# Kernel tuning notes

Measured on AMD Instinct MI355X. Metric: run time of the kernel, lower is better.

## Reference

```python
import jax, jax.numpy as jnp
import numpy as np


def setup_inputs() -> dict:
    key = jax.random.key(0)
    kq, kk, kv = jax.random.split(key, 3)
    B, H, S, D = 2, 16, 2048, 128
    return {
        "query_states": jax.random.normal(kq, (B, H, S, D), dtype=jnp.float32),
        "key_states": jax.random.normal(kk, (B, H, S, D), dtype=jnp.float32),
        "value_states": jax.random.normal(kv, (B, H, S, D), dtype=jnp.float32),
    }


def reference(query_states, key_states, value_states):
    # Faithful translation of CoreAttention.forward with attention_mask=None,
    # attention_dropout=0.0 (default, and dropout with p=0 is identity).
    B, H, Sq, D = query_states.shape
    Skv = key_states.shape[-2]
    scale = 1.0 / jnp.sqrt(jnp.asarray(D, dtype=query_states.dtype))
    # [B,H,Sq,Skv] score matrix (the module materializes this explicitly)
    attn_weights = jnp.einsum("bhqd,bhkd->bhqk", query_states, key_states) * scale
    # internal causal mask: triu(ones, diagonal=1) positions -> dtype min
    causal = jnp.triu(jnp.ones((Sq, Skv), dtype=bool), k=1)
    mask_value = jnp.finfo(attn_weights.dtype).min
    attn_weights = jnp.where(causal[None, None], mask_value, attn_weights)
    # torch does softmax in float64 then casts back; numerically stable fp32
    # softmax is equivalent to working precision here (jax x64 disabled).
    attn_weights = jax.nn.softmax(attn_weights, axis=-1).astype(query_states.dtype)
    attn_output = jnp.einsum("bhqk,bhkd->bhqd", attn_weights, value_states)
    return attn_output
```

## Files before the change

### kernel.cpp

```cpp
#include <hip/hip_runtime.h>
#include <hip/hip_bf16.h>
#include <stdint.h>

typedef __bf16  bf16x8 __attribute__((ext_vector_type(8)));
typedef __bf16  bf16x4 __attribute__((ext_vector_type(4)));
typedef float   f32x4  __attribute__((ext_vector_type(4)));
typedef uint32_t u32x4 __attribute__((ext_vector_type(4)));

#define S     2048
#define D     128
#define KVBLK 32
#define NQT   32
#define THR2  11.5415603f

__device__ __forceinline__ uint32_t cvt_pk(float lo, float hi2) {
    uint32_t u;
    asm("v_cvt_pk_bf16_f32 %0, %1, %2" : "=v"(u) : "v"(lo), "v"(hi2));
    return u;
}
__device__ __forceinline__ float exp2fast(float x) {
    return __builtin_amdgcn_exp2f(x);
}
__device__ __forceinline__ void gl2lds16(const void* g, void* l) {
    __builtin_amdgcn_global_load_lds(
        (const __attribute__((address_space(1))) void*)g,
        (__attribute__((address_space(3))) void*)l, 16, 0, 0);
}

__global__ __launch_bounds__(256) void pack_kv(
    const float* __restrict__ K, const float* __restrict__ V,
    __bf16* __restrict__ Kp, __bf16* __restrict__ Vp)
{
    const int bh = blockIdx.x, t = blockIdx.y;
    const int tid = threadIdx.x;
    const int kv0 = t * KVBLK;

    {
        const float* src = K + ((size_t)bh * S + kv0) * D;
        char* dst = (char*)Kp + ((size_t)(bh * 64 + t)) * 8192;
        #pragma unroll
        for (int cc = 0; cc < 2; ++cc) {
            const int c = cc * 256 + tid;
            const int row = c >> 4, col16 = c & 15;
            const float4 a = *reinterpret_cast<const float4*>(src + row * D + col16 * 8);
            const float4 b = *reinterpret_cast<const float4*>(src + row * D + col16 * 8 + 4);
            bf16x8 o;
            o[0]=(__bf16)a.x; o[1]=(__bf16)a.y; o[2]=(__bf16)a.z; o[3]=(__bf16)a.w;
            o[4]=(__bf16)b.x; o[5]=(__bf16)b.y; o[6]=(__bf16)b.z; o[7]=(__bf16)b.w;
            *reinterpret_cast<bf16x8*>(
                dst + row * 256 + ((col16 * 16) ^ ((row & 15) << 4))) = o;
        }
    }

    __shared__ __bf16 lds[32][136];
    {
        const float* src = V + ((size_t)bh * S + kv0) * D;
        #pragma unroll
        for (int it = 0; it < 4; ++it) {
            const int id = it * 256 + tid;
            const int row = id >> 5, c4 = id & 31;
            float4 v = *reinterpret_cast<const float4*>(src + row * D + c4 * 4);
            bf16x4 b4;
            b4[0]=(__bf16)v.x; b4[1]=(__bf16)v.y; b4[2]=(__bf16)v.z; b4[3]=(__bf16)v.w;
            *reinterpret_cast<bf16x4*>(&lds[row][c4 * 4]) = b4;
        }
    }
    __syncthreads();
    {
        char* dst = (char*)Vp + ((size_t)(bh * 64 + t)) * 8192;
        #pragma unroll
        for (int cc = 0; cc < 2; ++cc) {
            const int c = cc * 256 + tid;
            const int d = c >> 2, c8 = c & 3;
            bf16x8 o;
            #pragma unroll
            for (int k = 0; k < 8; ++k) o[k] = lds[c8 * 8 + k][d];
            const int addr = (d >> 1) * 128 +
                ((((d & 1) << 6) + c8 * 16) ^ (((d >> 1) & 3) << 4));
            *reinterpret_cast<bf16x8*>(dst + addr) = o;
        }
    }
}

__global__ __launch_bounds__(256, 4) void attn_fwd(
    const float* __restrict__ Q, const __bf16* __restrict__ Kp,
    const __bf16* __restrict__ Vp, float* __restrict__ O)
{
    const int bh = blockIdx.x;
    const int qt = (NQT - 1) - blockIdx.y;
    const int tid  = threadIdx.x;
    const int w    = tid >> 6;
    const int lane = tid & 63;
    const int r    = lane & 15;
    const int g    = lane >> 4;

    const float* Qh = Q + (size_t)bh * S * D;
    float*       Oh = O + (size_t)bh * S * D;
    const char*  Kbase = (const char*)Kp + (size_t)bh * 64 * 8192;
    const char*  Vbase = (const char*)Vp + (size_t)bh * 64 * 8192;

    const int q0w = qt * 64 + w * 16;

    __shared__ __align__(16) __bf16 K_sh[2][KVBLK * D];
    __shared__ __align__(16) __bf16 V_sh[2][D * KVBLK];

    const float scale = 0.08838834764831845f * 1.4426950408889634f;

    bf16x8 qfrag[4];
    {
        const float4* qp = reinterpret_cast<const float4*>(
            Qh + (size_t)(q0w + r) * D + g * 8);
        #pragma unroll
        for (int kb = 0; kb < 4; ++kb) {
            float4 a = qp[kb*8 + 0];
            float4 b = qp[kb*8 + 1];
            a.x*=scale; a.y*=scale; a.z*=scale; a.w*=scale;
            b.x*=scale; b.y*=scale; b.z*=scale; b.w*=scale;
            bf16x8 f;
            f[0]=(__bf16)a.x; f[1]=(__bf16)a.y; f[2]=(__bf16)a.z; f[3]=(__bf16)a.w;
            f[4]=(__bf16)b.x; f[5]=(__bf16)b.y; f[6]=(__bf16)b.z; f[7]=(__bf16)b.w;
            qfrag[kb] = f;
        }
    }

    auto STAGE = [&](int buf, int t) {
        const char* ks = Kbase + (size_t)t * 8192 + w * 1024 + lane * 16;
        const char* vs = Vbase + (size_t)t * 8192 + w * 1024 + lane * 16;
        char* kd = (char*)(&K_sh[buf][0]) + w * 1024;
        char* vd = (char*)(&V_sh[buf][0]) + w * 1024;
        gl2lds16(ks,        kd);
        gl2lds16(ks + 4096, kd + 4096);
        gl2lds16(vs,        vd);
        gl2lds16(vs + 4096, vd + 4096);
    };

    const f32x4 vzero = {0.f, 0.f, 0.f, 0.f};
    f32x4 acc_o[8];
    #pragma unroll
    for (int i = 0; i < 8; ++i) acc_o[i] = vzero;
    float m_run = -1e30f, l_run = 0.f;

    const int n_iter = 2 * qt + 2;
    const int my_max = (q0w + 15) >> 5;

    STAGE(0, 0);
    __syncthreads();
    int cur = 0;

    for (int t = 0; t < n_iter; ++t) {
        if (t + 1 < n_iter) STAGE(cur ^ 1, t + 1);

        if (t <= my_max) {
            const int kv0 = t * KVBLK;
            char* Kb = reinterpret_cast<char*>(&K_sh[cur][0]);
            char* Vb = reinterpret_cast<char*>(&V_sh[cur][0]);
            const bool alive1 = (kv0 + 16 <= q0w + 15);

            f32x4 st[2] = {vzero, vzero};
            __builtin_amdgcn_s_setprio(1);
            #pragma unroll
            for (int tt = 0; tt < 2; ++tt) {
                if (tt == 1 && !alive1) break;
                const int row = tt * 16 + r;
                #pragma unroll
                for (int kb = 0; kb < 4; ++kb) {
                    bf16x8 kf = *reinterpret_cast<const bf16x8*>(
                        Kb + row * 256 + ((kb*64 + g*16) ^ ((row & 15) << 4)));
                    st[tt] = __builtin_amdgcn_mfma_f32_16x16x32_bf16(
                        kf, qfrag[kb], st[tt], 0, 0, 0);
                }
            }
            __builtin_amdgcn_s_setprio(0);

            const int q = q0w + r;
            float pmax = -1e30f;
            #pragma unroll
            for (int tt = 0; tt < 2; ++tt) {
                if (tt == 1 && !alive1) break;
                if (kv0 + tt*16 + 15 > q0w) {
                    #pragma unroll
                    for (int jj = 0; jj < 4; ++jj)
                        if (kv0 + tt*16 + 4*g + jj > q) st[tt][jj] = -1e30f;
                }
                #pragma unroll
                for (int jj = 0; jj < 4; ++jj) pmax = fmaxf(pmax, st[tt][jj]);
            }
            pmax = fmaxf(pmax, __shfl_xor(pmax, 16));
            pmax = fmaxf(pmax, __shfl_xor(pmax, 32));

            if (__any(pmax > m_run + THR2)) {
                const float m_new = fmaxf(m_run, pmax);
                const float corr  = exp2fast(m_run - m_new);
                l_run *= corr; m_run = m_new;
                #pragma unroll
                for (int reg = 0; reg < 4; ++reg) {
                    const float cr = __shfl(corr, 4*g + reg);
                    #pragma unroll
                    for (int dt = 0; dt < 8; ++dt) acc_o[dt][reg] *= cr;
                }
            }

            float rowsum = 0.f;
            #pragma unroll
            for (int tt = 0; tt < 2; ++tt) {
                if (tt == 1 && !alive1) break;
                #pragma unroll
                for (int jj = 0; jj < 4; ++jj) {
                    const float p = exp2fast(st[tt][jj] - m_run);
                    st[tt][jj] = p;
                    rowsum += p;
                }
            }
            rowsum += __shfl_xor(rowsum, 16);
            rowsum += __shfl_xor(rowsum, 32);
            l_run += rowsum;

            const uint32_t p00 = cvt_pk(st[0][0], st[0][1]);
            const uint32_t p01 = cvt_pk(st[0][2], st[0][3]);
            const uint32_t p10 = alive1 ? cvt_pk(st[1][0], st[1][1]) : 0u;
            const uint32_t p11 = alive1 ? cvt_pk(st[1][2], st[1][3]) : 0u;
            const int sA = r + ((2 * (g & 1)) << 4);
            const int sB = r + ((2 * (g & 1) + 1) << 4);
            u32x4 words;
            {
                const uint32_t lo0 = (uint32_t)__shfl((int)p00, sA);
                const uint32_t hi0 = (uint32_t)__shfl((int)p10, sA);
                const uint32_t lo1 = (uint32_t)__shfl((int)p01, sA);
                const uint32_t hi1 = (uint32_t)__shfl((int)p11, sA);
                const uint32_t lo2 = (uint32_t)__shfl((int)p00, sB);
                const uint32_t hi2 = (uint32_t)__shfl((int)p10, sB);
                const uint32_t lo3 = (uint32_t)__shfl((int)p01, sB);
                const uint32_t hi3 = (uint32_t)__shfl((int)p11, sB);
                words[0] = (g & 2) ? hi0 : lo0;
                words[1] = (g & 2) ? hi1 : lo1;
                words[2] = (g & 2) ? hi2 : lo2;
                words[3] = (g & 2) ? hi3 : lo3;
            }
            const bf16x8 pa = __builtin_bit_cast(bf16x8, words);

            __builtin_amdgcn_s_setprio(1);
            #pragma unroll
            for (int dt = 0; dt < 8; ++dt) {
                const int d = dt * 16 + r;
                const int byte = (d >> 1) * 128 +
                    ((((d & 1) << 6) + (g << 4)) ^ (((d >> 1) & 3) << 4));
                bf16x8 vf = *reinterpret_cast<const bf16x8*>(Vb + byte);
                acc_o[dt] = __builtin_amdgcn_mfma_f32_16x16x32_bf16(
                    pa, vf, acc_o[dt], 0, 0, 0);
            }
            __builtin_amdgcn_s_setprio(0);
        }

        __syncthreads();
        cur ^= 1;
    }

    const float inv = 1.0f / l_run;
    #pragma unroll
    for (int reg = 0; reg < 4; ++reg) {
        const float iv = __shfl(inv, 4*g + reg);
        float* orow = Oh + (size_t)(q0w + 4*g + reg) * D + r;
        #pragma unroll
        for (int dt = 0; dt < 8; ++dt)
            orow[dt * 16] = acc_o[dt][reg] * iv;
    }
}

extern "C" void kernel_launch(void* const* d_in, const int* in_sizes, int n_in,
                              void* d_out, int out_size, void* d_ws, size_t ws_size,
                              hipStream_t stream) {
    const float* Q = (const float*)d_in[0];
    const float* K = (const float*)d_in[1];
    const float* V = (const float*)d_in[2];
    float* O = (float*)d_out;

    __bf16* Kp = (__bf16*)d_ws;
    __bf16* Vp = Kp + (size_t)32 * S * D;

    pack_kv<<<dim3(32, 64), 256, 0, stream>>>(K, V, Kp, Vp);
    attn_fwd<<<dim3(32, NQT), 256, 0, stream>>>(Q, Kp, Vp, O);
}
```

Baseline: 104.2 us.

## Pair high and low causal query tiles per block to balance work

Each block now handles two query tiles, one from the top and one from the bottom of the causal triangle. Both share each staged K/V tile from shared memory, so every block does roughly equal work and K/V loads are reused across the pair. The grid is halved and launch bounds drop to 2 waves per SIMD to make room for the doubled accumulators. The trade is lower occupancy and fewer blocks in exchange for load balance and less K/V traffic.

After: 104.9 us. Within noise of the previous version (+0.7%).

```diff
diff --git a/kernel.cpp b/kernel.cpp
--- a/kernel.cpp
+++ b/kernel.cpp
@@ -82,12 +82,14 @@
     }
 }
 
-__global__ __launch_bounds__(256, 4) void attn_fwd(
+__global__ __launch_bounds__(256, 2) void attn_fwd(
     const float* __restrict__ Q, const __bf16* __restrict__ Kp,
     const __bf16* __restrict__ Vp, float* __restrict__ O)
 {
     const int bh = blockIdx.x;
-    const int qt = (NQT - 1) - blockIdx.y;
+    const int y  = blockIdx.y;
+    const int qtH = NQT - 1 - y;
+    const int qtL = y;
     const int tid  = threadIdx.x;
     const int w    = tid >> 6;
     const int lane = tid & 63;
@@ -99,17 +101,17 @@
     const char*  Kbase = (const char*)Kp + (size_t)bh * 64 * 8192;
     const char*  Vbase = (const char*)Vp + (size_t)bh * 64 * 8192;
 
-    const int q0w = qt * 64 + w * 16;
+    const int q0H = qtH * 64 + w * 16;
+    const int q0L = qtL * 64 + w * 16;
 
     __shared__ __align__(16) __bf16 K_sh[2][KVBLK * D];
     __shared__ __align__(16) __bf16 V_sh[2][D * KVBLK];
 
     const float scale = 0.08838834764831845f * 1.4426950408889634f;
 
-    bf16x8 qfrag[4];
-    {
+    auto load_q = [&](int q0, bf16x8* qf) {
         const float4* qp = reinterpret_cast<const float4*>(
-            Qh + (size_t)(q0w + r) * D + g * 8);
+            Qh + (size_t)(q0 + r) * D + g * 8);
         #pragma unroll
         for (int kb = 0; kb < 4; ++kb) {
             float4 a = qp[kb*8 + 0];
@@ -119,9 +121,12 @@
             bf16x8 f;
             f[0]=(__bf16)a.x; f[1]=(__bf16)a.y; f[2]=(__bf16)a.z; f[3]=(__bf16)a.w;
             f[4]=(__bf16)b.x; f[5]=(__bf16)b.y; f[6]=(__bf16)b.z; f[7]=(__bf16)b.w;
-            qfrag[kb] = f;
-        }
-    }
+            qf[kb] = f;
+        }
+    };
+    bf16x8 qfH[4], qfL[4];
+    load_q(q0H, qfH);
+    load_q(q0L, qfL);
 
     auto STAGE = [&](int buf, int t) {
         const char* ks = Kbase + (size_t)t * 8192 + w * 1024 + lane * 16;
@@ -135,13 +140,115 @@
     };
 
     const f32x4 vzero = {0.f, 0.f, 0.f, 0.f};
-    f32x4 acc_o[8];
+    f32x4 accH[8], accL[8];
     #pragma unroll
-    for (int i = 0; i < 8; ++i) acc_o[i] = vzero;
-    float m_run = -1e30f, l_run = 0.f;
-
-    const int n_iter = 2 * qt + 2;
-    const int my_max = (q0w + 15) >> 5;
+    for (int i = 0; i < 8; ++i) { accH[i] = vzero; accL[i] = vzero; }
+    float mH = -1e30f, lH = 0.f, mL = -1e30f, lL = 0.f;
+
+    const int n_iter = 2 * qtH + 2;
+    const int maxH = (q0H + 15) >> 5;
+    const int maxL = (q0L + 15) >> 5;
+
+    auto stream_tile = [&](int t, int q0, const bf16x8* qf,
+                           f32x4* acc, float& m_run, float& l_run,
+                           char* Kb, char* Vb) {
+        const int kv0 = t * KVBLK;
+        const bool alive1 = (kv0 + 16 <= q0 + 15);
+
+        f32x4 st[2] = {vzero, vzero};
+        __builtin_amdgcn_s_setprio(1);
+        #pragma unroll
+        for (int tt = 0; tt < 2; ++tt) {
+            if (tt == 1 && !alive1) break;
+            const int row = tt * 16 + r;
+            #pragma unroll
+            for (int kb = 0; kb < 4; ++kb) {
+                bf16x8 kf = *reinterpret_cast<const bf16x8*>(
+                    Kb + row * 256 + ((kb*64 + g*16) ^ ((row & 15) << 4)));
+                st[tt] = __builtin_amdgcn_mfma_f32_16x16x32_bf16(
+                    kf, qf[kb], st[tt], 0, 0, 0);
+            }
+        }
+        __builtin_amdgcn_s_setprio(0);
+
+        const int q = q0 + r;
+        float pmax = -1e30f;
+        #pragma unroll
+        for (int tt = 0; tt < 2; ++tt) {
+            if (tt == 1 && !alive1) break;
+            if (kv0 + tt*16 + 15 > q0) {
+                #pragma unroll
+                for (int jj = 0; jj < 4; ++jj)
+                    if (kv0 + tt*16 + 4*g + jj > q) st[tt][jj] = -1e30f;
+            }
+            #pragma unroll
+            for (int jj = 0; jj < 4; ++jj) pmax = fmaxf(pmax, st[tt][jj]);
+        }
+        pmax = fmaxf(pmax, __shfl_xor(pmax, 16));
+        pmax = fmaxf(pmax, __shfl_xor(pmax, 32));
+
+        if (__any(pmax > m_run + THR2)) {
+            const float m_new = fmaxf(m_run, pmax);
+            const float corr  = exp2fast(m_run - m_new);
+            l_run *= corr; m_run = m_new;
+            #pragma unroll
+            for (int reg = 0; reg < 4; ++reg) {
+                const float cr = __shfl(corr, 4*g + reg);
+                #pragma unroll
+                for (int dt = 0; dt < 8; ++dt) acc[dt][reg] *= cr;
+            }
+        }
+
+        float rowsum = 0.f;
+        #pragma unroll
+        for (int tt = 0; tt < 2; ++tt) {
+            if (tt == 1 && !alive1) break;
+            #pragma unroll
+            for (int jj = 0; jj < 4; ++jj) {
+                const float p = exp2fast(st[tt][jj] - m_run);
+                st[tt][jj] = p;
+                rowsum += p;
+            }
+        }
+        rowsum += __shfl_xor(rowsum, 16);
+        rowsum += __shfl_xor(rowsum, 32);
+        l_run += rowsum;
+
+        const uint32_t p00 = cvt_pk(st[0][0], st[0][1]);
+        const uint32_t p01 = cvt_pk(st[0][2], st[0][3]);
+        const uint32_t p10 = alive1 ? cvt_pk(st[1][0], st[1][1]) : 0u;
+        const uint32_t p11 = alive1 ? cvt_pk(st[1][2], st[1][3]) : 0u;
+        const int sA = r + ((2 * (g & 1)) << 4);
+        const int sB = r + ((2 * (g & 1) + 1) << 4);
+        u32x4 words;
+        {
+            const uint32_t lo0 = (uint32_t)__shfl((int)p00, sA);
+            const uint32_t hi0 = (uint32_t)__shfl((int)p10, sA);
+            const uint32_t lo1 = (uint32_t)__shfl((int)p01, sA);
+            const uint32_t hi1 = (uint32_t)__shfl((int)p11, sA);
+            const uint32_t lo2 = (uint32_t)__shfl((int)p00, sB);
+            const uint32_t hi2 = (uint32_t)__shfl((int)p10, sB);
+            const uint32_t lo3 = (uint32_t)__shfl((int)p01, sB);
+            const uint32_t hi3 = (uint32_t)__shfl((int)p11, sB);
+            words[0] = (g & 2) ? hi0 : lo0;
+            words[1] = (g & 2) ? hi1 : lo1;
+            words[2] = (g & 2) ? hi2 : lo2;
+            words[3] = (g & 2) ? hi3 : lo3;
+        }
+        const bf16x8 pa = __builtin_bit_cast(bf16x8, words);
+
+        __builtin_amdgcn_s_setprio(1);
+        #pragma unroll
+        for (int dt = 0; dt < 8; ++dt) {
+            const int d = dt * 16 + r;
+            const int byte = (d >> 1) * 128 +
+                ((((d & 1) << 6) + (g << 4)) ^ (((d >> 1) & 3) << 4));
+            bf16x8 vf = *reinterpret_cast<const bf16x8*>(Vb + byte);
+            acc[dt] = __builtin_amdgcn_mfma_f32_16x16x32_bf16(
+                pa, vf, acc[dt], 0, 0, 0);
+        }
+        __builtin_amdgcn_s_setprio(0);
+    };
 
     STAGE(0, 0);
     __syncthreads();
@@ -149,121 +256,27 @@
 
     for (int t = 0; t < n_iter; ++t) {
         if (t + 1 < n_iter) STAGE(cur ^ 1, t + 1);
-
-        if (t <= my_max) {
-            const int kv0 = t * KVBLK;
-            char* Kb = reinterpret_cast<char*>(&K_sh[cur][0]);
-            char* Vb = reinterpret_cast<char*>(&V_sh[cur][0]);
-            const bool alive1 = (kv0 + 16 <= q0w + 15);
-
-            f32x4 st[2] = {vzero, vzero};
-            __builtin_amdgcn_s_setprio(1);
-            #pragma unroll
-            for (int tt = 0; tt < 2; ++tt) {
-                if (tt == 1 && !alive1) break;
-                const int row = tt * 16 + r;
-                #pragma unroll
-                for (int kb = 0; kb < 4; ++kb) {
-                    bf16x8 kf = *reinterpret_cast<const bf16x8*>(
-                        Kb + row * 256 + ((kb*64 + g*16) ^ ((row & 15) << 4)));
-                    st[tt] = __builtin_amdgcn_mfma_f32_16x16x32_bf16(
-                        kf, qfrag[kb], st[tt], 0, 0, 0);
-                }
-            }
-            __builtin_amdgcn_s_setprio(0);
-
-            const int q = q0w + r;
-            float pmax = -1e30f;
-            #pragma unroll
-            for (int tt = 0; tt < 2; ++tt) {
-                if (tt == 1 && !alive1) break;
-                if (kv0 + tt*16 + 15 > q0w) {
-                    #pragma unroll
-                    for (int jj = 0; jj < 4; ++jj)
-                        if (kv0 + tt*16 + 4*g + jj > q) st[tt][jj] = -1e30f;
-                }
-                #pragma unroll
-                for (int jj = 0; jj < 4; ++jj) pmax = fmaxf(pmax, st[tt][jj]);
-            }
-            pmax = fmaxf(pmax, __shfl_xor(pmax, 16));
-            pmax = fmaxf(pmax, __shfl_xor(pmax, 32));
-
-            if (__any(pmax > m_run + THR2)) {
-                const float m_new = fmaxf(m_run, pmax);
-                const float corr  = exp2fast(m_run - m_new);
-                l_run *= corr; m_run = m_new;
-                #pragma unroll
-                for (int reg = 0; reg < 4; ++reg) {
-                    const float cr = __shfl(corr, 4*g + reg);
-                    #pragma unroll
-                    for (int dt = 0; dt < 8; ++dt) acc_o[dt][reg] *= cr;
-                }
-            }
-
-            float rowsum = 0.f;
-            #pragma unroll
-            for (int tt = 0; tt < 2; ++tt) {
-                if (tt == 1 && !alive1) break;
-                #pragma unroll
-                for (int jj = 0; jj < 4; ++jj) {
-                    const float p = exp2fast(st[tt][jj] - m_run);
-                    st[tt][jj] = p;
-                    rowsum += p;
-                }
-            }
-            rowsum += __shfl_xor(rowsum, 16);
-            rowsum += __shfl_xor(rowsum, 32);
-            l_run += rowsum;
-
-            const uint32_t p00 = cvt_pk(st[0][0], st[0][1]);
-            const uint32_t p01 = cvt_pk(st[0][2], st[0][3]);
-            const uint32_t p10 = alive1 ? cvt_pk(st[1][0], st[1][1]) : 0u;
-            const uint32_t p11 = alive1 ? cvt_pk(st[1][2], st[1][3]) : 0u;
-            const int sA = r + ((2 * (g & 1)) << 4);
-            const int sB = r + ((2 * (g & 1) + 1) << 4);
-            u32x4 words;
-            {
-                const uint32_t lo0 = (uint32_t)__shfl((int)p00, sA);
-                const uint32_t hi0 = (uint32_t)__shfl((int)p10, sA);
-                const uint32_t lo1 = (uint32_t)__shfl((int)p01, sA);
-                const uint32_t hi1 = (uint32_t)__shfl((int)p11, sA);
-                const uint32_t lo2 = (uint32_t)__shfl((int)p00, sB);
-                const uint32_t hi2 = (uint32_t)__shfl((int)p10, sB);
-                const uint32_t lo3 = (uint32_t)__shfl((int)p01, sB);
-                const uint32_t hi3 = (uint32_t)__shfl((int)p11, sB);
-                words[0] = (g & 2) ? hi0 : lo0;
-                words[1] = (g & 2) ? hi1 : lo1;
-                words[2] = (g & 2) ? hi2 : lo2;
-                words[3] = (g & 2) ? hi3 : lo3;
-            }
-            const bf16x8 pa = __builtin_bit_cast(bf16x8, words);
-
-            __builtin_amdgcn_s_setprio(1);
-            #pragma unroll
-            for (int dt = 0; dt < 8; ++dt) {
-                const int d = dt * 16 + r;
-                const int byte = (d >> 1) * 128 +
-                    ((((d & 1) << 6) + (g << 4)) ^ (((d >> 1) & 3) << 4));
-                bf16x8 vf = *reinterpret_cast<const bf16x8*>(Vb + byte);
-                acc_o[dt] = __builtin_amdgcn_mfma_f32_16x16x32_bf16(
-                    pa, vf, acc_o[dt], 0, 0, 0);
-            }
-            __builtin_amdgcn_s_setprio(0);
-        }
-
+        char* Kb = reinterpret_cast<char*>(&K_sh[cur][0]);
+        char* Vb = reinterpret_cast<char*>(&V_sh[cur][0]);
+        if (t <= maxL) stream_tile(t, q0L, qfL, accL, mL, lL, Kb, Vb);
+        if (t <= maxH) stream_tile(t, q0H, qfH, accH, mH, lH, Kb, Vb);
         __syncthreads();
         cur ^= 1;
     }
 
-    const float inv = 1.0f / l_run;
-    #pragma unroll
-    for (int reg = 0; reg < 4; ++reg) {
-        const float iv = __shfl(inv, 4*g + reg);
-        float* orow = Oh + (size_t)(q0w + 4*g + reg) * D + r;
-        #pragma unroll
-        for (int dt = 0; dt < 8; ++dt)
-            orow[dt * 16] = acc_o[dt][reg] * iv;
-    }
+    auto epilogue = [&](int q0, f32x4* acc, float l_run) {
+        const float inv = 1.0f / l_run;
+        #pragma unroll
+        for (int reg = 0; reg < 4; ++reg) {
+            const float iv = __shfl(inv, 4*g + reg);
+            float* orow = Oh + (size_t)(q0 + 4*g + reg) * D + r;
+            #pragma unroll
+            for (int dt = 0; dt < 8; ++dt)
+                orow[dt * 16] = acc[dt][reg] * iv;
+        }
+    };
+    epilogue(q0H, accH, lH);
+    epilogue(q0L, accL, lL);
 }
 
 extern "C" void kernel_launch(void* const* d_in, const int* in_sizes, int n_in,
@@ -278,5 +291,5 @@
     __bf16* Vp = Kp + (size_t)32 * S * D;
 
     pack_kv<<<dim3(32, 64), 256, 0, stream>>>(K, V, Kp, Vp);
-    attn_fwd<<<dim3(32, NQT), 256, 0, stream>>>(Q, Kp, Vp, O);
-}
+    attn_fwd<<<dim3(32, 16), 256, 0, stream>>>(Q, Kp, Vp, O);
+}
```

## Switch attention to 32x32x16 MFMA with 128-row Q tiles and 64-wide KV blocks

Applied to the files above, without the earlier changes.

Rewrites the attention kernel to use 32x32x16 bf16 MFMA instructions. Each wave now owns 32 query rows and each workgroup 128, with KV staged in 64-row blocks. The K/V pack layout and swizzles are changed to match the new fragment shapes, and the P-to-A-operand shuffle becomes a simpler xor-32 exchange. The aim is more reuse per LDS load and fewer cross-lane shuffles. In exchange the kernel needs more registers and runs at lower occupancy (launch bounds 2), and launches half as many workgroups with coarser causal tiles.

New measurement: 93.80 us. 1.11x faster.

```diff
diff --git a/kernel.cpp b/kernel.cpp
--- a/kernel.cpp
+++ b/kernel.cpp
@@ -4,14 +4,15 @@
 
 typedef __bf16  bf16x8 __attribute__((ext_vector_type(8)));
 typedef __bf16  bf16x4 __attribute__((ext_vector_type(4)));
-typedef float   f32x4  __attribute__((ext_vector_type(4)));
+typedef float   f32x16 __attribute__((ext_vector_type(16)));
 typedef uint32_t u32x4 __attribute__((ext_vector_type(4)));
 
 #define S     2048
 #define D     128
-#define KVBLK 32
-#define NQT   32
+#define TKV   64
+#define NQB   16
 #define THR2  11.5415603f
+#define KROW(reg) ((((reg) & 3) + 8 * ((reg) >> 2)) + 4 * hi)
 
 __device__ __forceinline__ uint32_t cvt_pk(float lo, float hi2) {
     uint32_t u;
@@ -33,11 +34,12 @@
 {
     const int bh = blockIdx.x, t = blockIdx.y;
     const int tid = threadIdx.x;
-    const int kv0 = t * KVBLK;
+    const int kv0 = t * 32;
+    const int pair = t >> 1, half = t & 1;
 
     {
         const float* src = K + ((size_t)bh * S + kv0) * D;
-        char* dst = (char*)Kp + ((size_t)(bh * 64 + t)) * 8192;
+        char* dst = (char*)Kp + ((size_t)(bh * 32 + pair)) * 16384 + half * 8192;
         #pragma unroll
         for (int cc = 0; cc < 2; ++cc) {
             const int c = cc * 256 + tid;
@@ -67,7 +69,7 @@
     }
     __syncthreads();
     {
-        char* dst = (char*)Vp + ((size_t)(bh * 64 + t)) * 8192;
+        char* dst = (char*)Vp + ((size_t)(bh * 32 + pair)) * 16384;
         #pragma unroll
         for (int cc = 0; cc < 2; ++cc) {
             const int c = cc * 256 + tid;
@@ -75,73 +77,74 @@
             bf16x8 o;
             #pragma unroll
             for (int k = 0; k < 8; ++k) o[k] = lds[c8 * 8 + k][d];
-            const int addr = (d >> 1) * 128 +
-                ((((d & 1) << 6) + c8 * 16) ^ (((d >> 1) & 3) << 4));
+            const int addr = d * 128 + (((half * 4 + c8) ^ (d & 7)) << 4);
             *reinterpret_cast<bf16x8*>(dst + addr) = o;
         }
     }
 }
 
-__global__ __launch_bounds__(256, 4) void attn_fwd(
+__global__ __launch_bounds__(256, 2) void attn_fwd(
     const float* __restrict__ Q, const __bf16* __restrict__ Kp,
     const __bf16* __restrict__ Vp, float* __restrict__ O)
 {
     const int bh = blockIdx.x;
-    const int qt = (NQT - 1) - blockIdx.y;
+    const int qt = (NQB - 1) - blockIdx.y;
     const int tid  = threadIdx.x;
     const int w    = tid >> 6;
     const int lane = tid & 63;
-    const int r    = lane & 15;
-    const int g    = lane >> 4;
+    const int c    = lane & 31;
+    const int hi   = lane >> 5;
 
     const float* Qh = Q + (size_t)bh * S * D;
     float*       Oh = O + (size_t)bh * S * D;
-    const char*  Kbase = (const char*)Kp + (size_t)bh * 64 * 8192;
-    const char*  Vbase = (const char*)Vp + (size_t)bh * 64 * 8192;
-
-    const int q0w = qt * 64 + w * 16;
-
-    __shared__ __align__(16) __bf16 K_sh[2][KVBLK * D];
-    __shared__ __align__(16) __bf16 V_sh[2][D * KVBLK];
+    const char*  Kbase = (const char*)Kp + (size_t)bh * 32 * 16384;
+    const char*  Vbase = (const char*)Vp + (size_t)bh * 32 * 16384;
+
+    const int q0w = qt * 128 + w * 32;
+
+    __shared__ __align__(16) __bf16 K_sh[2][TKV * D];
+    __shared__ __align__(16) __bf16 V_sh[2][D * TKV];
 
     const float scale = 0.08838834764831845f * 1.4426950408889634f;
 
-    bf16x8 qfrag[4];
-    {
-        const float4* qp = reinterpret_cast<const float4*>(
-            Qh + (size_t)(q0w + r) * D + g * 8);
-        #pragma unroll
-        for (int kb = 0; kb < 4; ++kb) {
-            float4 a = qp[kb*8 + 0];
-            float4 b = qp[kb*8 + 1];
+    bf16x8 qfrag[8];
+    {
+        const float* qrow = Qh + (size_t)(q0w + c) * D;
+        #pragma unroll
+        for (int ks = 0; ks < 8; ++ks) {
+            const int d0 = ks * 16 + hi * 8;
+            float4 a = *reinterpret_cast<const float4*>(qrow + d0);
+            float4 b = *reinterpret_cast<const float4*>(qrow + d0 + 4);
             a.x*=scale; a.y*=scale; a.z*=scale; a.w*=scale;
             b.x*=scale; b.y*=scale; b.z*=scale; b.w*=scale;
             bf16x8 f;
             f[0]=(__bf16)a.x; f[1]=(__bf16)a.y; f[2]=(__bf16)a.z; f[3]=(__bf16)a.w;
             f[4]=(__bf16)b.x; f[5]=(__bf16)b.y; f[6]=(__bf16)b.z; f[7]=(__bf16)b.w;
-            qfrag[kb] = f;
-        }
-    }
-
-    auto STAGE = [&](int buf, int t) {
-        const char* ks = Kbase + (size_t)t * 8192 + w * 1024 + lane * 16;
-        const char* vs = Vbase + (size_t)t * 8192 + w * 1024 + lane * 16;
-        char* kd = (char*)(&K_sh[buf][0]) + w * 1024;
-        char* vd = (char*)(&V_sh[buf][0]) + w * 1024;
-        gl2lds16(ks,        kd);
-        gl2lds16(ks + 4096, kd + 4096);
-        gl2lds16(vs,        vd);
-        gl2lds16(vs + 4096, vd + 4096);
+            qfrag[ks] = f;
+        }
+    }
+
+    auto STAGE = [&](int buf, int t64) {
+        const char* ks = Kbase + (size_t)t64 * 16384 + w * 4096 + lane * 16;
+        const char* vs = Vbase + (size_t)t64 * 16384 + w * 4096 + lane * 16;
+        char* kd = (char*)(&K_sh[buf][0]) + w * 4096;
+        char* vd = (char*)(&V_sh[buf][0]) + w * 4096;
+        #pragma unroll
+        for (int i = 0; i < 4; ++i) {
+            gl2lds16(ks + i * 1024, kd + i * 1024);
+            gl2lds16(vs + i * 1024, vd + i * 1024);
+        }
     };
 
-    const f32x4 vzero = {0.f, 0.f, 0.f, 0.f};
-    f32x4 acc_o[8];
+    f32x16 acc_o[4];
     #pragma unroll
-    for (int i = 0; i < 8; ++i) acc_o[i] = vzero;
+    for (int dt = 0; dt < 4; ++dt)
+        #pragma unroll
+        for (int i = 0; i < 16; ++i) acc_o[dt][i] = 0.f;
     float m_run = -1e30f, l_run = 0.f;
 
     const int n_iter = 2 * qt + 2;
-    const int my_max = (q0w + 15) >> 5;
+    const int my_max = (q0w + 31) >> 6;
 
     STAGE(0, 0);
     __syncthreads();
@@ -151,41 +154,43 @@
         if (t + 1 < n_iter) STAGE(cur ^ 1, t + 1);
 
         if (t <= my_max) {
-            const int kv0 = t * KVBLK;
+            const int kv0 = t * TKV;
             char* Kb = reinterpret_cast<char*>(&K_sh[cur][0]);
             char* Vb = reinterpret_cast<char*>(&V_sh[cur][0]);
-            const bool alive1 = (kv0 + 16 <= q0w + 15);
-
-            f32x4 st[2] = {vzero, vzero};
+            const bool alive1 = (kv0 + 32 <= q0w + 31);
+
+            f32x16 st[2];
             __builtin_amdgcn_s_setprio(1);
             #pragma unroll
-            for (int tt = 0; tt < 2; ++tt) {
-                if (tt == 1 && !alive1) break;
-                const int row = tt * 16 + r;
-                #pragma unroll
-                for (int kb = 0; kb < 4; ++kb) {
+            for (int sub = 0; sub < 2; ++sub) {
+                #pragma unroll
+                for (int i = 0; i < 16; ++i) st[sub][i] = 0.f;
+                if (sub == 1 && !alive1) break;
+                const int row = sub * 32 + c;
+                #pragma unroll
+                for (int ks = 0; ks < 8; ++ks) {
                     bf16x8 kf = *reinterpret_cast<const bf16x8*>(
-                        Kb + row * 256 + ((kb*64 + g*16) ^ ((row & 15) << 4)));
-                    st[tt] = __builtin_amdgcn_mfma_f32_16x16x32_bf16(
-                        kf, qfrag[kb], st[tt], 0, 0, 0);
+                        Kb + row * 256 + (((ks*2 + hi) ^ (row & 15)) << 4));
+                    st[sub] = __builtin_amdgcn_mfma_f32_32x32x16_bf16(
+                        kf, qfrag[ks], st[sub], 0, 0, 0);
                 }
             }
             __builtin_amdgcn_s_setprio(0);
 
-            const int q = q0w + r;
+            const int q = q0w + c;
             float pmax = -1e30f;
             #pragma unroll
-            for (int tt = 0; tt < 2; ++tt) {
-                if (tt == 1 && !alive1) break;
-                if (kv0 + tt*16 + 15 > q0w) {
+            for (int sub = 0; sub < 2; ++sub) {
+                if (sub == 1 && !alive1) break;
+                if (kv0 + sub*32 + 31 > q0w) {
                     #pragma unroll
-                    for (int jj = 0; jj < 4; ++jj)
-                        if (kv0 + tt*16 + 4*g + jj > q) st[tt][jj] = -1e30f;
-                }
-                #pragma unroll
-                for (int jj = 0; jj < 4; ++jj) pmax = fmaxf(pmax, st[tt][jj]);
-            }
-            pmax = fmaxf(pmax, __shfl_xor(pmax, 16));
+                    for (int reg = 0; reg < 16; ++reg)
+                        if (kv0 + sub*32 + KROW(reg) > q) st[sub][reg] = -1e30f;
+                }
+                #pragma unroll
+                for (int reg = 0; reg < 16; ++reg)
+                    pmax = fmaxf(pmax, st[sub][reg]);
+            }
             pmax = fmaxf(pmax, __shfl_xor(pmax, 32));
 
             if (__any(pmax > m_run + THR2)) {
@@ -193,62 +198,56 @@
                 const float corr  = exp2fast(m_run - m_new);
                 l_run *= corr; m_run = m_new;
                 #pragma unroll
-                for (int reg = 0; reg < 4; ++reg) {
-                    const float cr = __shfl(corr, 4*g + reg);
+                for (int reg = 0; reg < 16; ++reg) {
+                    const float cr = __shfl(corr, KROW(reg));
                     #pragma unroll
-                    for (int dt = 0; dt < 8; ++dt) acc_o[dt][reg] *= cr;
+                    for (int dt = 0; dt < 4; ++dt) acc_o[dt][reg] *= cr;
                 }
             }
 
             float rowsum = 0.f;
             #pragma unroll
-            for (int tt = 0; tt < 2; ++tt) {
-                if (tt == 1 && !alive1) break;
-                #pragma unroll
-                for (int jj = 0; jj < 4; ++jj) {
-                    const float p = exp2fast(st[tt][jj] - m_run);
-                    st[tt][jj] = p;
+            for (int sub = 0; sub < 2; ++sub) {
+                if (sub == 1 && !alive1) break;
+                #pragma unroll
+                for (int reg = 0; reg < 16; ++reg) {
+                    const float p = exp2fast(st[sub][reg] - m_run);
+                    st[sub][reg] = p;
                     rowsum += p;
                 }
             }
-            rowsum += __shfl_xor(rowsum, 16);
             rowsum += __shfl_xor(rowsum, 32);
             l_run += rowsum;
 
-            const uint32_t p00 = cvt_pk(st[0][0], st[0][1]);
-            const uint32_t p01 = cvt_pk(st[0][2], st[0][3]);
-            const uint32_t p10 = alive1 ? cvt_pk(st[1][0], st[1][1]) : 0u;
-            const uint32_t p11 = alive1 ? cvt_pk(st[1][2], st[1][3]) : 0u;
-            const int sA = r + ((2 * (g & 1)) << 4);
-            const int sB = r + ((2 * (g & 1) + 1) << 4);
-            u32x4 words;
-            {
-                const uint32_t lo0 = (uint32_t)__shfl((int)p00, sA);
-                const uint32_t hi0 = (uint32_t)__shfl((int)p10, sA);
-                const uint32_t lo1 = (uint32_t)__shfl((int)p01, sA);
-                const uint32_t hi1 = (uint32_t)__shfl((int)p11, sA);
-                const uint32_t lo2 = (uint32_t)__shfl((int)p00, sB);
-                const uint32_t hi2 = (uint32_t)__shfl((int)p10, sB);
-                const uint32_t lo3 = (uint32_t)__shfl((int)p01, sB);
-                const uint32_t hi3 = (uint32_t)__shfl((int)p11, sB);
-                words[0] = (g & 2) ? hi0 : lo0;
-                words[1] = (g & 2) ? hi1 : lo1;
-                words[2] = (g & 2) ? hi2 : lo2;
-                words[3] = (g & 2) ? hi3 : lo3;
-            }
-            const bf16x8 pa = __builtin_bit_cast(bf16x8, words);
-
-            __builtin_amdgcn_s_setprio(1);
-            #pragma unroll
-            for (int dt = 0; dt < 8; ++dt) {
-                const int d = dt * 16 + r;
-                const int byte = (d >> 1) * 128 +
-                    ((((d & 1) << 6) + (g << 4)) ^ (((d >> 1) & 3) << 4));
-                bf16x8 vf = *reinterpret_cast<const bf16x8*>(Vb + byte);
-                acc_o[dt] = __builtin_amdgcn_mfma_f32_16x16x32_bf16(
-                    pa, vf, acc_o[dt], 0, 0, 0);
-            }
-            __builtin_amdgcn_s_setprio(0);
+            #pragma unroll
+            for (int ks = 0; ks < 4; ++ks) {
+                if (kv0 + ks*16 > q0w + 31) break;
+                const int sub = ks >> 1, k1 = (ks & 1) * 8;
+                const uint32_t pkA0 = cvt_pk(st[sub][k1+0], st[sub][k1+1]);
+                const uint32_t pkA1 = cvt_pk(st[sub][k1+2], st[sub][k1+3]);
+                const uint32_t pkB0 = cvt_pk(st[sub][k1+4], st[sub][k1+5]);
+                const uint32_t pkB1 = cvt_pk(st[sub][k1+6], st[sub][k1+7]);
+                const uint32_t rA0 = (uint32_t)__shfl_xor((int)pkA0, 32);
+                const uint32_t rA1 = (uint32_t)__shfl_xor((int)pkA1, 32);
+                const uint32_t rB0 = (uint32_t)__shfl_xor((int)pkB0, 32);
+                const uint32_t rB1 = (uint32_t)__shfl_xor((int)pkB1, 32);
+                u32x4 words;
+                words[0] = hi ? rB0 : pkA0;
+                words[1] = hi ? rB1 : pkA1;
+                words[2] = hi ? pkB0 : rA0;
+                words[3] = hi ? pkB1 : rA1;
+                const bf16x8 pa = __builtin_bit_cast(bf16x8, words);
+                __builtin_amdgcn_s_setprio(1);
+                #pragma unroll
+                for (int dt = 0; dt < 4; ++dt) {
+                    const int d = dt * 32 + c;
+                    bf16x8 vf = *reinterpret_cast<const bf16x8*>(
+                        Vb + d * 128 + (((ks*2 + hi) ^ (d & 7)) << 4));
+                    acc_o[dt] = __builtin_amdgcn_mfma_f32_32x32x16_bf16(
+                        pa, vf, acc_o[dt], 0, 0, 0);
+                }
+                __builtin_amdgcn_s_setprio(0);
+            }
         }
 
         __syncthreads();
@@ -257,12 +256,12 @@
 
     const float inv = 1.0f / l_run;
     #pragma unroll
-    for (int reg = 0; reg < 4; ++reg) {
-        const float iv = __shfl(inv, 4*g + reg);
-        float* orow = Oh + (size_t)(q0w + 4*g + reg) * D + r;
-        #pragma unroll
-        for (int dt = 0; dt < 8; ++dt)
-            orow[dt * 16] = acc_o[dt][reg] * iv;
+    for (int reg = 0; reg < 16; ++reg) {
+        const float iv = __shfl(inv, KROW(reg));
+        float* orow = Oh + (size_t)(q0w + KROW(reg)) * D + c;
+        #pragma unroll
+        for (int dt = 0; dt < 4; ++dt)
+            orow[dt * 32] = acc_o[dt][reg] * iv;
     }
 }
 
@@ -278,5 +277,5 @@
     __bf16* Vp = Kp + (size_t)32 * S * D;
 
     pack_kv<<<dim3(32, 64), 256, 0, stream>>>(K, V, Kp, Vp);
-    attn_fwd<<<dim3(32, NQT), 256, 0, stream>>>(Q, Kp, Vp, O);
-}
+    attn_fwd<<<dim3(32, NQB), 256, 0, stream>>>(Q, Kp, Vp, O);
+}
```
